# Performance work log

Hardware: AMD Instinct MI355X
Metric: run time of the kernel (lower is better)

The kernel has to match this reference:

```python
import jax, jax.numpy as jnp
import numpy as np

NUM_HEADS = 32
NUM_KV_HEADS = 8
HEAD_DIM = 128
ROPE_BASE = 10000.0


def rotate_half(x):
    half = x.shape[-1] // 2
    x1, x2 = x[..., :half], x[..., half:]
    return jnp.concatenate((-x2, x1), axis=-1)


def rope_cos_sin(position_ids, head_dim, dtype):
    # inv_freq: [head_dim/2]
    inv_freq = 1.0 / (ROPE_BASE ** (jnp.arange(0, head_dim, 2, dtype=jnp.float32) / head_dim))
    freqs = position_ids.astype(jnp.float32)[..., None] * inv_freq  # [B, S, hd/2]
    emb = jnp.concatenate((freqs, freqs), axis=-1)                  # [B, S, hd]
    # add head axis -> [B, 1, S, hd]
    return jnp.cos(emb)[:, None].astype(dtype), jnp.sin(emb)[:, None].astype(dtype)


def setup_inputs() -> dict:
    key = jax.random.key(0)
    k_x, k_q, k_k, k_v, k_o = jax.random.split(key, 5)
    B, S, H = 1, 2048, 4096
    w_scale = 0.02
    return {
        "hidden_states": jax.random.normal(k_x, (B, S, H), dtype=jnp.float32),
        "position_ids": jnp.broadcast_to(jnp.arange(S, dtype=jnp.int32), (B, S)),
        "Wq": jax.random.normal(k_q, (NUM_HEADS * HEAD_DIM, H), dtype=jnp.float32) * w_scale,
        "Wk": jax.random.normal(k_k, (NUM_KV_HEADS * HEAD_DIM, H), dtype=jnp.float32) * w_scale,
        "Wv": jax.random.normal(k_v, (NUM_KV_HEADS * HEAD_DIM, H), dtype=jnp.float32) * w_scale,
        "Wo": jax.random.normal(k_o, (H, NUM_HEADS * HEAD_DIM), dtype=jnp.float32) * w_scale,
    }


def reference(hidden_states, position_ids, Wq, Wk, Wv, Wo):
    B, S, H = hidden_states.shape
    n_rep = NUM_HEADS // NUM_KV_HEADS

    # projections (torch Linear: y = x @ W.T), reshape to [B, heads, S, hd]
    q = (hidden_states @ Wq.T).reshape(B, S, NUM_HEADS, HEAD_DIM).transpose(0, 2, 1, 3)
    k = (hidden_states @ Wk.T).reshape(B, S, NUM_KV_HEADS, HEAD_DIM).transpose(0, 2, 1, 3)
    v = (hidden_states @ Wv.T).reshape(B, S, NUM_KV_HEADS, HEAD_DIM).transpose(0, 2, 1, 3)

    cos, sin = rope_cos_sin(position_ids, HEAD_DIM, hidden_states.dtype)
    q = q * cos + rotate_half(q) * sin
    k = k * cos + rotate_half(k) * sin

    # repeat_kv: GQA expansion to [B, NUM_HEADS, S, hd]
    k = jnp.repeat(k, n_rep, axis=1)
    v = jnp.repeat(v, n_rep, axis=1)

    scale = 1.0 / jnp.sqrt(jnp.asarray(HEAD_DIM, dtype=hidden_states.dtype))
    scores = jnp.einsum('bhqd,bhkd->bhqk', q, k) * scale  # [B, H, S, S]

    # causal additive mask
    causal = jnp.tril(jnp.ones((S, S), dtype=bool))
    scores = jnp.where(causal[None, None], scores, jnp.finfo(scores.dtype).min)

    probs = jax.nn.softmax(scores, axis=-1)
    attn = jnp.einsum('bhqk,bhkd->bhqd', probs, v)         # [B, H, S, hd]
    attn = attn.transpose(0, 2, 1, 3).reshape(B, S, NUM_HEADS * HEAD_DIM)
    return attn @ Wo.T
```

## Files before the change

### kernel.cpp

```cpp
#include <hip/hip_runtime.h>
#include <hip/hip_bf16.h>
#include <stdint.h>

typedef __bf16 bf16;
typedef __attribute__((ext_vector_type(8))) __bf16 bf16x8;
typedef __attribute__((ext_vector_type(4))) __bf16 bf16x4;
typedef __attribute__((ext_vector_type(4))) float f32x4;
typedef __attribute__((ext_vector_type(16))) float f32x16;

#define S_LEN 2048
#define HDIM  4096
#define NQH   32
#define NKVH  8
#define DHEAD 128
#define QKVN  6144
#define KOFF  4096
#define VOFF  5120

__device__ __forceinline__ void gload_lds16(const bf16* g, bf16* l) {
  __builtin_amdgcn_global_load_lds(
      (const __attribute__((address_space(1))) unsigned int*)g,
      (__attribute__((address_space(3))) unsigned int*)l, 16, 0, 0);
}

__global__ __launch_bounds__(256) void cvt_f32_bf16(const float* __restrict__ in,
                                                    bf16* __restrict__ out, int n4) {
  int i = blockIdx.x * 256 + threadIdx.x;
  if (i >= n4) return;
  float4 v = ((const float4*)in)[i];
  bf16x4 ov = {(bf16)v.x, (bf16)v.y, (bf16)v.z, (bf16)v.w};
  *(bf16x4*)&out[(size_t)i * 4] = ov;
}

__global__ __launch_bounds__(256) void rope_table(const int* __restrict__ pos,
                                                  float* __restrict__ tab) {
  int idx = blockIdx.x * 256 + threadIdx.x;
  int i = idx & 63, s = idx >> 6;
  float p = (float)pos[s];
  float invf = powf(10000.0f, -(float)i * (1.0f / 64.0f));
  float ang = p * invf;
  tab[idx * 2]     = cosf(ang);
  tab[idx * 2 + 1] = sinf(ang);
}

__global__ __launch_bounds__(256) void rope_apply(bf16* __restrict__ QKV,
                                                  const float* __restrict__ tab) {
  int idx = blockIdx.x * 256 + threadIdx.x;
  int dp = idx & 63;
  int t = idx >> 6;
  int head = t % 40;
  int s = t / 40;
  float c  = tab[(s * 64 + dp) * 2];
  float sn = tab[(s * 64 + dp) * 2 + 1];
  size_t base = (size_t)s * QKVN + head * DHEAD;
  float x0 = (float)QKV[base + dp];
  float x1 = (float)QKV[base + 64 + dp];
  QKV[base + dp]      = (bf16)(x0 * c - x1 * sn);
  QKV[base + 64 + dp] = (bf16)(x1 * c + x0 * sn);
}

__global__ __launch_bounds__(256) void transpose_v(const bf16* __restrict__ QKV,
                                                   bf16* __restrict__ Vt) {
  __shared__ bf16 t[64][72];
  int tid = threadIdx.x;
  int bs = blockIdx.x * 64, bc = blockIdx.y * 64;
  int sl = tid >> 3, cb = (tid & 7) * 8;
#pragma unroll
  for (int ss = 0; ss < 64; ss += 32) {
    int s = sl + ss;
    *(bf16x8*)&t[s][cb] = *(const bf16x8*)&QKV[(size_t)(bs + s) * QKVN + VOFF + bc + cb];
  }
  __syncthreads();
  int cl = tid >> 3, sb = (tid & 7) * 8;
#pragma unroll
  for (int cc = 0; cc < 64; cc += 32) {
    int c = cl + cc;
    bf16x8 v;
#pragma unroll
    for (int k = 0; k < 8; ++k) v[k] = t[sb + k][c];
    *(bf16x8*)&Vt[(size_t)(bc + c) * S_LEN + bs + sb] = v;
  }
}

template <typename OutT>
__global__ __launch_bounds__(256) void gemm_bt(const bf16* __restrict__ A,
                                               const bf16* __restrict__ B,
                                               OutT* __restrict__ C,
                                               int M, int N, int K) {
  __shared__ bf16 At[128 * 64];
  __shared__ bf16 Bt[128 * 64];
  const int tid = threadIdx.x;
  const int w = tid >> 6, lane = tid & 63;
  const int r = lane & 15, g = lane >> 4;
  const int bm = blockIdx.y * 128, bn = blockIdx.x * 128;
  const int wm = (w >> 1) * 64, wn = (w & 1) * 64;
  f32x4 acc[4][4];
#pragma unroll
  for (int i = 0; i < 4; ++i)
#pragma unroll
    for (int j = 0; j < 4; ++j) acc[i][j] = (f32x4){0.f, 0.f, 0.f, 0.f};

  const int chunk0 = w * 256 + lane;

  for (int k0 = 0; k0 < K; k0 += 64) {
#pragma unroll
    for (int i = 0; i < 4; ++i) {
      int chunk = chunk0 + i * 64;
      int row = chunk >> 3, c8 = chunk & 7;
      int cs = ((c8 ^ (row & 7)) << 3) + k0;
      gload_lds16(&A[(size_t)(bm + row) * K + cs], &At[(w * 4 + i) * 512]);
      gload_lds16(&B[(size_t)(bn + row) * K + cs], &Bt[(w * 4 + i) * 512]);
    }
    __syncthreads();
#pragma unroll
    for (int ks = 0; ks < 2; ++ks) {
      bf16x8 af[4], bfr[4];
#pragma unroll
      for (int mi = 0; mi < 4; ++mi) {
        int row = wm + mi * 16 + r;
        af[mi] = *(const bf16x8*)&At[row * 64 + ((((ks << 2) + g) ^ (row & 7)) << 3)];
      }
#pragma unroll
      for (int nj = 0; nj < 4; ++nj) {
        int row = wn + nj * 16 + r;
        bfr[nj] = *(const bf16x8*)&Bt[row * 64 + ((((ks << 2) + g) ^ (row & 7)) << 3)];
      }
#pragma unroll
      for (int mi = 0; mi < 4; ++mi)
#pragma unroll
        for (int nj = 0; nj < 4; ++nj)
          acc[mi][nj] = __builtin_amdgcn_mfma_f32_16x16x32_bf16(af[mi], bfr[nj],
                                                                acc[mi][nj], 0, 0, 0);
    }
    __syncthreads();
  }
#pragma unroll
  for (int mi = 0; mi < 4; ++mi)
#pragma unroll
    for (int nj = 0; nj < 4; ++nj)
#pragma unroll
      for (int j = 0; j < 4; ++j) {
        int row = bm + wm + mi * 16 + g * 4 + j;
        int col = bn + wn + nj * 16 + r;
        C[(size_t)row * N + col] = (OutT)acc[mi][nj][j];
      }
}

__global__ __launch_bounds__(64, 2) void attn_kernel(const bf16* __restrict__ QKV,
                                                     const bf16* __restrict__ Vt,
                                                     bf16* __restrict__ Oout) {
  const int lane = threadIdx.x & 63;
  const int l31 = lane & 31, hi = lane >> 5;
  const int qblk = 63 - (blockIdx.x >> 5);
  const int h = blockIdx.x & 31;
  const int kvh = h >> 2;
  const int q0 = qblk * 32;
  const float scale = 0.12751746f;

  bf16x8 qf[8];
#pragma unroll
  for (int k8 = 0; k8 < 8; ++k8) {
    bf16x8 raw = *(const bf16x8*)&QKV[(size_t)(q0 + l31) * QKVN + h * DHEAD + k8 * 16 + hi * 8];
#pragma unroll
    for (int e = 0; e < 8; ++e) qf[k8][e] = (bf16)((float)raw[e] * scale);
  }

  f32x16 o[4];
#pragma unroll
  for (int t = 0; t < 4; ++t)
#pragma unroll
    for (int r = 0; r < 16; ++r) o[t][r] = 0.f;
  float m_run = -1e30f, l_run = 0.f;

  auto loadK = [&](bf16x8 (&kd)[8], int kv0) {
#pragma unroll
    for (int k8 = 0; k8 < 8; ++k8)
      kd[k8] = *(const bf16x8*)&QKV[(size_t)(kv0 + l31) * QKVN + KOFF +
                                    kvh * DHEAD + k8 * 16 + hi * 8];
  };

  auto process = [&](bf16x8 (&kc)[8], bf16x8 (&kn)[8], int kv0, bool pre, bool diag) {
    bf16x8 vf[8];
#pragma unroll
    for (int t = 0; t < 4; ++t) {
      const bf16* vb = &Vt[(size_t)(kvh * DHEAD + t * 32 + l31) * S_LEN + kv0 + hi * 8];
      vf[2 * t]     = *(const bf16x8*)vb;
      vf[2 * t + 1] = *(const bf16x8*)(vb + 16);
    }
    f32x16 st;
#pragma unroll
    for (int r = 0; r < 16; ++r) st[r] = 0.f;
#pragma unroll
    for (int k8 = 0; k8 < 8; ++k8)
      st = __builtin_amdgcn_mfma_f32_32x32x16_bf16(kc[k8], qf[k8], st, 0, 0, 0);
    if (pre) loadK(kn, kv0 + 32);
    if (diag) {
#pragma unroll
      for (int r = 0; r < 16; ++r) {
        int kvr = (r & 3) + 8 * (r >> 2) + 4 * hi;
        if (kvr > l31) st[r] = -1e30f;
      }
    }
    float pmax = st[0];
#pragma unroll
    for (int r = 1; r < 16; ++r) pmax = fmaxf(pmax, st[r]);
    pmax = fmaxf(pmax, __shfl_xor(pmax, 32));
    if (!__all(pmax - m_run <= 8.0f)) {
      float mnew = fmaxf(m_run, pmax);
      float corr = exp2f(m_run - mnew);
      m_run = mnew;
      l_run *= corr;
#pragma unroll
      for (int r = 0; r < 16; ++r) {
        float cr = __shfl(corr, (r & 3) + 8 * (r >> 2) + 4 * hi);
        o[0][r] *= cr; o[1][r] *= cr; o[2][r] *= cr; o[3][r] *= cr;
      }
    }
    float p[16], rs = 0.f;
#pragma unroll
    for (int r = 0; r < 16; ++r) { p[r] = exp2f(st[r] - m_run); rs += p[r]; }
    rs += __shfl_xor(rs, 32);
    l_run += rs;
    float sp[16];
#pragma unroll
    for (int i = 0; i < 16; ++i) sp[i] = __shfl_xor(p[i], 32);
    bf16x8 pf0, pf1;
#pragma unroll
    for (int e = 0; e < 4; ++e) {
      pf0[e]     = (bf16)(hi ? sp[4 + e]  : p[e]);
      pf0[e + 4] = (bf16)(hi ? p[4 + e]   : sp[e]);
      pf1[e]     = (bf16)(hi ? sp[12 + e] : p[8 + e]);
      pf1[e + 4] = (bf16)(hi ? p[12 + e]  : sp[8 + e]);
    }
#pragma unroll
    for (int t = 0; t < 4; ++t) {
      o[t] = __builtin_amdgcn_mfma_f32_32x32x16_bf16(pf0, vf[2 * t],     o[t], 0, 0, 0);
      o[t] = __builtin_amdgcn_mfma_f32_32x32x16_bf16(pf1, vf[2 * t + 1], o[t], 0, 0, 0);
    }
  };

  const int nt = qblk + 1;
  bf16x8 kfA[8], kfB[8];
  loadK(kfA, 0);
  int t = 0;
  while (true) {
    process(kfA, kfB, t * 32, t + 1 < nt, t == nt - 1);
    ++t; if (t >= nt) break;
    process(kfB, kfA, t * 32, t + 1 < nt, t == nt - 1);
    ++t; if (t >= nt) break;
  }

  float linv = 1.0f / l_run;
#pragma unroll
  for (int r = 0; r < 16; ++r) {
    int qloc = (r & 3) + 8 * (r >> 2) + 4 * hi;
    float li = __shfl(linv, qloc);
    size_t row = (size_t)(q0 + qloc) * HDIM + h * DHEAD;
#pragma unroll
    for (int t2 = 0; t2 < 4; ++t2)
      Oout[row + t2 * 32 + l31] = (bf16)(o[t2][r] * li);
  }
}

extern "C" void kernel_launch(void* const* d_in, const int* in_sizes, int n_in,
                              void* d_out, int out_size, void* d_ws, size_t ws_size,
                              hipStream_t stream) {
  const float* X   = (const float*)d_in[0];
  const int*   pos = (const int*)d_in[1];
  const float* Wq  = (const float*)d_in[2];
  const float* Wk  = (const float*)d_in[3];
  const float* Wv  = (const float*)d_in[4];
  const float* Wo  = (const float*)d_in[5];
  float* out = (float*)d_out;
  char* ws = (char*)d_ws;

  size_t off = 0;
  bf16* Xb    = (bf16*)(ws + off); off += (size_t)2048 * 4096 * 2;
  bf16* Wqkvb = (bf16*)(ws + off); off += (size_t)6144 * 4096 * 2;
  bf16* Wob   = (bf16*)(ws + off); off += (size_t)4096 * 4096 * 2;
  bf16* QKV   = (bf16*)(ws + off); off += (size_t)2048 * 6144 * 2;
  bf16* Vt    = (bf16*)(ws + off); off += (size_t)1024 * 2048 * 2;
  bf16* attnb = (bf16*)(ws + off); off += (size_t)2048 * 4096 * 2;
  float* tab  = (float*)(ws + off); off += (size_t)2048 * 64 * 2 * 4;

  cvt_f32_bf16<<<2048 * 4096 / 4 / 256, 256, 0, stream>>>(X, Xb, 2048 * 4096 / 4);
  cvt_f32_bf16<<<4096 * 4096 / 4 / 256, 256, 0, stream>>>(Wq, Wqkvb, 4096 * 4096 / 4);
  cvt_f32_bf16<<<1024 * 4096 / 4 / 256, 256, 0, stream>>>(Wk, Wqkvb + (size_t)4096 * 4096,
                                                          1024 * 4096 / 4);
  cvt_f32_bf16<<<1024 * 4096 / 4 / 256, 256, 0, stream>>>(Wv, Wqkvb + (size_t)5120 * 4096,
                                                          1024 * 4096 / 4);
  cvt_f32_bf16<<<4096 * 4096 / 4 / 256, 256, 0, stream>>>(Wo, Wob, 4096 * 4096 / 4);
  rope_table<<<2048 * 64 / 256, 256, 0, stream>>>(pos, tab);
  gemm_bt<bf16><<<dim3(QKVN / 128, 2048 / 128), 256, 0, stream>>>(Xb, Wqkvb, QKV,
                                                                  2048, QKVN, 4096);
  rope_apply<<<2048 * 40 * 64 / 256, 256, 0, stream>>>(QKV, tab);
  transpose_v<<<dim3(2048 / 64, 1024 / 64), 256, 0, stream>>>(QKV, Vt);
  attn_kernel<<<2048, 64, 0, stream>>>(QKV, Vt, attnb);
  gemm_bt<float><<<dim3(4096 / 128, 2048 / 128), 256, 0, stream>>>(attnb, Wob, out,
                                                                   2048, 4096, 4096);
}
```

Measured before the change: 421.0 us.

## Split attention KV range into two partitions with a merge kernel

Each causal attention block's KV tiles are split in half across two workgroups, which write partial outputs plus max and sum statistics. A new merge kernel combines them into the final attention output. The aim is more parallelism and better load balance for the long-tail query blocks, with launch bounds raised to 4 waves and s_setprio around the MFMA sections. In exchange it adds an extra kernel launch, bf16 partial-output traffic, and reuses the already-consumed weight buffer as scratch.

Result: slower. 858.7 us (+104.0%).

```diff
diff --git a/kernel.cpp b/kernel.cpp
--- a/kernel.cpp
+++ b/kernel.cpp
@@ -146,24 +146,27 @@
       }
 }
 
-__global__ __launch_bounds__(64, 2) void attn_kernel(const bf16* __restrict__ QKV,
+__global__ __launch_bounds__(64, 4) void attn_kernel(const bf16* __restrict__ QKV,
                                                      const bf16* __restrict__ Vt,
-                                                     bf16* __restrict__ Oout) {
+                                                     bf16* __restrict__ Opart,
+                                                     float* __restrict__ Mpart,
+                                                     float* __restrict__ Lpart) {
   const int lane = threadIdx.x & 63;
   const int l31 = lane & 31, hi = lane >> 5;
-  const int qblk = 63 - (blockIdx.x >> 5);
-  const int h = blockIdx.x & 31;
-  const int kvh = h >> 2;
+  const int bx = blockIdx.x;
+  const int kvh = bx & 7;
+  const int hq = (bx >> 3) & 3;
+  const int s = (bx >> 5) & 1;
+  const int qblk = 63 - (bx >> 6);
+  const int h = kvh * 4 + hq;
   const int q0 = qblk * 32;
+  const int pid = ((h * 64 + qblk) * 2 + s);
   const float scale = 0.12751746f;
 
-  bf16x8 qf[8];
-#pragma unroll
-  for (int k8 = 0; k8 < 8; ++k8) {
-    bf16x8 raw = *(const bf16x8*)&QKV[(size_t)(q0 + l31) * QKVN + h * DHEAD + k8 * 16 + hi * 8];
-#pragma unroll
-    for (int e = 0; e < 8; ++e) qf[k8][e] = (bf16)((float)raw[e] * scale);
-  }
+  const int nt = qblk + 1;
+  const int h0 = (nt + 1) >> 1;
+  const int t0 = s ? h0 : 0;
+  const int t1 = s ? nt : h0;
 
   f32x16 o[4];
 #pragma unroll
@@ -172,93 +175,139 @@
     for (int r = 0; r < 16; ++r) o[t][r] = 0.f;
   float m_run = -1e30f, l_run = 0.f;
 
-  auto loadK = [&](bf16x8 (&kd)[8], int kv0) {
-#pragma unroll
-    for (int k8 = 0; k8 < 8; ++k8)
-      kd[k8] = *(const bf16x8*)&QKV[(size_t)(kv0 + l31) * QKVN + KOFF +
-                                    kvh * DHEAD + k8 * 16 + hi * 8];
-  };
-
-  auto process = [&](bf16x8 (&kc)[8], bf16x8 (&kn)[8], int kv0, bool pre, bool diag) {
-    bf16x8 vf[8];
-#pragma unroll
-    for (int t = 0; t < 4; ++t) {
-      const bf16* vb = &Vt[(size_t)(kvh * DHEAD + t * 32 + l31) * S_LEN + kv0 + hi * 8];
-      vf[2 * t]     = *(const bf16x8*)vb;
-      vf[2 * t + 1] = *(const bf16x8*)(vb + 16);
+  if (t0 < t1) {
+    bf16x8 qf[8];
+#pragma unroll
+    for (int k8 = 0; k8 < 8; ++k8) {
+      bf16x8 raw = *(const bf16x8*)&QKV[(size_t)(q0 + l31) * QKVN + h * DHEAD + k8 * 16 + hi * 8];
+#pragma unroll
+      for (int e = 0; e < 8; ++e) qf[k8][e] = (bf16)((float)raw[e] * scale);
     }
-    f32x16 st;
-#pragma unroll
-    for (int r = 0; r < 16; ++r) st[r] = 0.f;
-#pragma unroll
-    for (int k8 = 0; k8 < 8; ++k8)
-      st = __builtin_amdgcn_mfma_f32_32x32x16_bf16(kc[k8], qf[k8], st, 0, 0, 0);
-    if (pre) loadK(kn, kv0 + 32);
-    if (diag) {
-#pragma unroll
-      for (int r = 0; r < 16; ++r) {
-        int kvr = (r & 3) + 8 * (r >> 2) + 4 * hi;
-        if (kvr > l31) st[r] = -1e30f;
-      }
+
+    auto loadK = [&](bf16x8 (&kd)[8], int kv0) {
+#pragma unroll
+      for (int k8 = 0; k8 < 8; ++k8)
+        kd[k8] = *(const bf16x8*)&QKV[(size_t)(kv0 + l31) * QKVN + KOFF +
+                                      kvh * DHEAD + k8 * 16 + hi * 8];
+    };
+
+    auto process = [&](bf16x8 (&kc)[8], bf16x8 (&kn)[8], int kv0, bool pre, bool diag) {
+      bf16x8 vf[8];
+#pragma unroll
+      for (int t = 0; t < 4; ++t) {
+        const bf16* vb = &Vt[(size_t)(kvh * DHEAD + t * 32 + l31) * S_LEN + kv0 + hi * 8];
+        vf[2 * t]     = *(const bf16x8*)vb;
+        vf[2 * t + 1] = *(const bf16x8*)(vb + 16);
+      }
+      f32x16 st;
+#pragma unroll
+      for (int r = 0; r < 16; ++r) st[r] = 0.f;
+      __builtin_amdgcn_s_setprio(1);
+#pragma unroll
+      for (int k8 = 0; k8 < 8; ++k8)
+        st = __builtin_amdgcn_mfma_f32_32x32x16_bf16(kc[k8], qf[k8], st, 0, 0, 0);
+      __builtin_amdgcn_s_setprio(0);
+      if (pre) loadK(kn, kv0 + 32);
+      if (diag) {
+#pragma unroll
+        for (int r = 0; r < 16; ++r) {
+          int kvr = (r & 3) + 8 * (r >> 2) + 4 * hi;
+          if (kvr > l31) st[r] = -1e30f;
+        }
+      }
+      float pmax = st[0];
+#pragma unroll
+      for (int r = 1; r < 16; ++r) pmax = fmaxf(pmax, st[r]);
+      pmax = fmaxf(pmax, __shfl_xor(pmax, 32));
+      if (!__all(pmax - m_run <= 8.0f)) {
+        float mnew = fmaxf(m_run, pmax);
+        float corr = exp2f(m_run - mnew);
+        m_run = mnew;
+        l_run *= corr;
+#pragma unroll
+        for (int r = 0; r < 16; ++r) {
+          float cr = __shfl(corr, (r & 3) + 8 * (r >> 2) + 4 * hi);
+          o[0][r] *= cr; o[1][r] *= cr; o[2][r] *= cr; o[3][r] *= cr;
+        }
+      }
+      float p[16], rs = 0.f;
+#pragma unroll
+      for (int r = 0; r < 16; ++r) { p[r] = exp2f(st[r] - m_run); rs += p[r]; }
+      rs += __shfl_xor(rs, 32);
+      l_run += rs;
+      float sp[16];
+#pragma unroll
+      for (int i = 0; i < 16; ++i) sp[i] = __shfl_xor(p[i], 32);
+      bf16x8 pf0, pf1;
+#pragma unroll
+      for (int e = 0; e < 4; ++e) {
+        pf0[e]     = (bf16)(hi ? sp[4 + e]  : p[e]);
+        pf0[e + 4] = (bf16)(hi ? p[4 + e]   : sp[e]);
+        pf1[e]     = (bf16)(hi ? sp[12 + e] : p[8 + e]);
+        pf1[e + 4] = (bf16)(hi ? p[12 + e]  : sp[8 + e]);
+      }
+      __builtin_amdgcn_s_setprio(1);
+#pragma unroll
+      for (int t = 0; t < 4; ++t) {
+        o[t] = __builtin_amdgcn_mfma_f32_32x32x16_bf16(pf0, vf[2 * t],     o[t], 0, 0, 0);
+        o[t] = __builtin_amdgcn_mfma_f32_32x32x16_bf16(pf1, vf[2 * t + 1], o[t], 0, 0, 0);
+      }
+      __builtin_amdgcn_s_setprio(0);
+    };
+
+    bf16x8 kfA[8], kfB[8];
+    loadK(kfA, t0 * 32);
+    int t = t0;
+    while (true) {
+      process(kfA, kfB, t * 32, t + 1 < t1, t == nt - 1);
+      ++t; if (t >= t1) break;
+      process(kfB, kfA, t * 32, t + 1 < t1, t == nt - 1);
+      ++t; if (t >= t1) break;
     }
-    float pmax = st[0];
-#pragma unroll
-    for (int r = 1; r < 16; ++r) pmax = fmaxf(pmax, st[r]);
-    pmax = fmaxf(pmax, __shfl_xor(pmax, 32));
-    if (!__all(pmax - m_run <= 8.0f)) {
-      float mnew = fmaxf(m_run, pmax);
-      float corr = exp2f(m_run - mnew);
-      m_run = mnew;
-      l_run *= corr;
-#pragma unroll
-      for (int r = 0; r < 16; ++r) {
-        float cr = __shfl(corr, (r & 3) + 8 * (r >> 2) + 4 * hi);
-        o[0][r] *= cr; o[1][r] *= cr; o[2][r] *= cr; o[3][r] *= cr;
-      }
-    }
-    float p[16], rs = 0.f;
-#pragma unroll
-    for (int r = 0; r < 16; ++r) { p[r] = exp2f(st[r] - m_run); rs += p[r]; }
-    rs += __shfl_xor(rs, 32);
-    l_run += rs;
-    float sp[16];
-#pragma unroll
-    for (int i = 0; i < 16; ++i) sp[i] = __shfl_xor(p[i], 32);
-    bf16x8 pf0, pf1;
-#pragma unroll
-    for (int e = 0; e < 4; ++e) {
-      pf0[e]     = (bf16)(hi ? sp[4 + e]  : p[e]);
-      pf0[e + 4] = (bf16)(hi ? p[4 + e]   : sp[e]);
-      pf1[e]     = (bf16)(hi ? sp[12 + e] : p[8 + e]);
-      pf1[e + 4] = (bf16)(hi ? p[12 + e]  : sp[8 + e]);
-    }
-#pragma unroll
-    for (int t = 0; t < 4; ++t) {
-      o[t] = __builtin_amdgcn_mfma_f32_32x32x16_bf16(pf0, vf[2 * t],     o[t], 0, 0, 0);
-      o[t] = __builtin_amdgcn_mfma_f32_32x32x16_bf16(pf1, vf[2 * t + 1], o[t], 0, 0, 0);
-    }
-  };
-
-  const int nt = qblk + 1;
-  bf16x8 kfA[8], kfB[8];
-  loadK(kfA, 0);
-  int t = 0;
-  while (true) {
-    process(kfA, kfB, t * 32, t + 1 < nt, t == nt - 1);
-    ++t; if (t >= nt) break;
-    process(kfB, kfA, t * 32, t + 1 < nt, t == nt - 1);
-    ++t; if (t >= nt) break;
-  }
-
-  float linv = 1.0f / l_run;
+  }
+
+  float linv = (l_run > 0.f) ? 1.0f / l_run : 0.f;
+  if (hi == 0) {
+    Mpart[pid * 32 + l31] = m_run;
+    Lpart[pid * 32 + l31] = l_run;
+  }
 #pragma unroll
   for (int r = 0; r < 16; ++r) {
     int qloc = (r & 3) + 8 * (r >> 2) + 4 * hi;
     float li = __shfl(linv, qloc);
-    size_t row = (size_t)(q0 + qloc) * HDIM + h * DHEAD;
+    size_t row = (size_t)pid * (32 * DHEAD) + (size_t)qloc * DHEAD;
 #pragma unroll
     for (int t2 = 0; t2 < 4; ++t2)
-      Oout[row + t2 * 32 + l31] = (bf16)(o[t2][r] * li);
+      Opart[row + t2 * 32 + l31] = (bf16)(o[t2][r] * li);
+  }
+}
+
+__global__ __launch_bounds__(256) void attn_merge(const bf16* __restrict__ Opart,
+                                                  const float* __restrict__ Mpart,
+                                                  const float* __restrict__ Lpart,
+                                                  bf16* __restrict__ Oout) {
+  const int bx = blockIdx.x;
+  const int h = bx >> 6, qblk = bx & 63;
+  const int tid = threadIdx.x;
+  const int r = tid >> 3, cseg = (tid & 7) * 16;
+  const int pid0 = bx * 2, pid1 = pid0 + 1;
+  float m0 = Mpart[pid0 * 32 + r], m1 = Mpart[pid1 * 32 + r];
+  float l0 = Lpart[pid0 * 32 + r], l1 = Lpart[pid1 * 32 + r];
+  float M = fmaxf(m0, m1);
+  float w0 = l0 * exp2f(m0 - M), w1 = l1 * exp2f(m1 - M);
+  float inv = 1.0f / (w0 + w1);
+  w0 *= inv; w1 *= inv;
+  size_t src0 = (size_t)pid0 * (32 * DHEAD) + (size_t)r * DHEAD + cseg;
+  size_t src1 = (size_t)pid1 * (32 * DHEAD) + (size_t)r * DHEAD + cseg;
+  size_t dst = (size_t)(qblk * 32 + r) * HDIM + h * DHEAD + cseg;
+#pragma unroll
+  for (int half = 0; half < 2; ++half) {
+    bf16x8 a = *(const bf16x8*)&Opart[src0 + half * 8];
+    bf16x8 b = *(const bf16x8*)&Opart[src1 + half * 8];
+    bf16x8 out;
+#pragma unroll
+    for (int e = 0; e < 8; ++e) out[e] = (bf16)(w0 * (float)a[e] + w1 * (float)b[e]);
+    *(bf16x8*)&Oout[dst + half * 8] = out;
   }
 }
 
@@ -282,6 +331,10 @@
   bf16* Vt    = (bf16*)(ws + off); off += (size_t)1024 * 2048 * 2;
   bf16* attnb = (bf16*)(ws + off); off += (size_t)2048 * 4096 * 2;
   float* tab  = (float*)(ws + off); off += (size_t)2048 * 64 * 2 * 4;
+
+  bf16*  Opart = (bf16*)Wqkvb;
+  float* Mpart = (float*)((char*)Wqkvb + (size_t)4096 * 32 * 128 * 2);
+  float* Lpart = Mpart + (size_t)4096 * 32;
 
   cvt_f32_bf16<<<2048 * 4096 / 4 / 256, 256, 0, stream>>>(X, Xb, 2048 * 4096 / 4);
   cvt_f32_bf16<<<4096 * 4096 / 4 / 256, 256, 0, stream>>>(Wq, Wqkvb, 4096 * 4096 / 4);
@@ -295,7 +348,8 @@
                                                                   2048, QKVN, 4096);
   rope_apply<<<2048 * 40 * 64 / 256, 256, 0, stream>>>(QKV, tab);
   transpose_v<<<dim3(2048 / 64, 1024 / 64), 256, 0, stream>>>(QKV, Vt);
-  attn_kernel<<<2048, 64, 0, stream>>>(QKV, Vt, attnb);
+  attn_kernel<<<4096, 64, 0, stream>>>(QKV, Vt, Opart, Mpart, Lpart);
+  attn_merge<<<2048, 256, 0, stream>>>(Opart, Mpart, Lpart, attnb);
   gemm_bt<float><<<dim3(4096 / 128, 2048 / 128), 256, 0, stream>>>(attnb, Wob, out,
                                                                    2048, 4096, 4096);
 }
```
